# Kernel optimization log

Hardware: AMD Instinct MI355X
Metric: run time of the kernel (lower is better)

Reference implementation:

```python
import jax, jax.numpy as jnp
import numpy as np

N, E, D, H, L, G, C = 50000, 800000, 128, 128, 3, 128, 10
BN_EPS = 1e-5


def setup_inputs() -> dict:
    key = jax.random.key(0)
    ks = jax.random.split(key, 16)
    inp = {
        "x": jax.random.normal(ks[0], (N, D), dtype=jnp.float32),
        "node_centrality": jax.random.uniform(ks[1], (N,), dtype=jnp.float32),
        "edge_centrality": jax.random.uniform(ks[2], (E,), dtype=jnp.float32),
        # stacked per-layer MLP params (in == hidden so stackable)
        "W1": jax.random.normal(ks[3], (L, D, H), dtype=jnp.float32) * 0.05,
        "b1": jnp.zeros((L, H), dtype=jnp.float32),
        "g1": jnp.ones((L, H), dtype=jnp.float32),
        "be1": jnp.zeros((L, H), dtype=jnp.float32),
        "W2": jax.random.normal(ks[4], (L, H, H), dtype=jnp.float32) * 0.05,
        "b2": jnp.zeros((L, H), dtype=jnp.float32),
        "Wc": jax.random.normal(ks[5], (H, C), dtype=jnp.float32) * 0.05,
        "bc": jnp.zeros((C,), dtype=jnp.float32),
        "edge_index": jax.random.randint(ks[6], (2, E), 0, N, dtype=jnp.int64),
        "batch": jnp.sort(jax.random.randint(ks[7], (N,), 0, G, dtype=jnp.int64)),
    }
    return inp


def _gin_forward(x, node_centrality, edge_centrality, W1, b1, g1, be1, W2, b2, Wc, bc, edge_index, batch):
    src, dst = edge_index[0], edge_index[1]  # x_j = x[src], aggregate at dst
    ec = edge_centrality[:, None]
    nc = node_centrality[:, None]
    for l in range(L):
        # message: gather + scale by edge centrality; aggr='add': scatter-add
        msg = x[src] * ec                                      # [E, H]
        agg = jax.ops.segment_sum(msg, dst, num_segments=N)    # [N, H]
        h = agg * nc + x                                       # (1 + eps) * x_r, eps = 0
        # MLP([in, hidden, hidden]): Linear -> BatchNorm(train) -> ReLU -> Linear
        h = h @ W1[l] + b1[l]
        mu = h.mean(axis=0)
        var = h.var(axis=0)  # biased, matches BN training stats
        h = (h - mu) * jax.lax.rsqrt(var + BN_EPS) * g1[l] + be1[l]
        h = jax.nn.relu(h)
        h = h @ W2[l] + b2[l]
        x = jax.nn.relu(h)  # outer .relu() in GIN.forward
    # global mean pool over graphs
    sums = jax.ops.segment_sum(x, batch, num_segments=G)           # [G, H]
    cnt = jax.ops.segment_sum(jnp.ones((N,), x.dtype), batch, num_segments=G)
    pooled = sums / jnp.maximum(cnt, 1.0)[:, None]
    return pooled @ Wc + bc  # [G, C]


def reference(x, edge_index, batch, node_centrality, edge_centrality, W1, b1, g1, be1, W2, b2, Wc, bc):
    return _gin_forward(x, node_centrality, edge_centrality, W1, b1, g1, be1, W2, b2, Wc, bc, edge_index, batch)
```

## Files before the change

### kernel.cpp

```cpp
#include <hip/hip_runtime.h>
#include <hip/hip_fp16.h>

#define Nn 50000
#define Ee 800000
#define HD 128
#define Ll 3
#define Gg 128
#define Cc 10
#define BN_EPS 1e-5f
#define NBLK1 782
#define PPAD 800
#define NSCB 49

typedef __attribute__((ext_vector_type(8))) __bf16 bf16x8;
typedef __attribute__((ext_vector_type(4))) __bf16 bf16x4;
typedef __attribute__((ext_vector_type(4))) float f32x4;

__global__ void k_deg(const int* __restrict__ dst, int* __restrict__ deg) {
  int i = blockIdx.x * blockDim.x + threadIdx.x;
  int base = i * 4;
  if (base >= Ee) return;
#pragma unroll
  for (int j = 0; j < 4; ++j) {
    int e = base + j;
    if (e < Ee) atomicAdd(&deg[dst[e]], 1);
  }
}

__global__ void k_scan1(const int* __restrict__ deg, int* __restrict__ offs,
                        int* __restrict__ bsum) {
  __shared__ int b0[1024], b1[1024];
  int tid = threadIdx.x;
  int i = blockIdx.x * 1024 + tid;
  int v = (i < Nn) ? deg[i] : 0;
  int* cur = b0; int* nxt = b1;
  cur[tid] = v;
  __syncthreads();
  for (int off = 1; off < 1024; off <<= 1) {
    int s = cur[tid] + ((tid >= off) ? cur[tid - off] : 0);
    nxt[tid] = s;
    __syncthreads();
    int* t = cur; cur = nxt; nxt = t;
  }
  if (i < Nn) offs[i] = cur[tid] - v;
  if (tid == 1023) bsum[blockIdx.x] = cur[1023];
}

__global__ void k_scan2(const int* __restrict__ bsum, int* __restrict__ carry) {
  int lane = threadIdx.x;
  int v = (lane < NSCB) ? bsum[lane] : 0;
  int s = v;
  for (int off = 1; off < 64; off <<= 1) {
    int t = __shfl_up(s, off, 64);
    if (lane >= off) s += t;
  }
  if (lane < NSCB) carry[lane] = s - v;
}

__global__ void k_scan3(const int* __restrict__ carry, int* __restrict__ offs,
                        int* __restrict__ cursor) {
  int i = blockIdx.x * 1024 + threadIdx.x;
  if (i < Nn) {
    int o = offs[i] + carry[blockIdx.x];
    offs[i] = o; cursor[i] = o;
  }
  if (i == 0) offs[Nn] = Ee;
}

__global__ void k_fill(const int* __restrict__ src, const int* __restrict__ dst,
                       const float* __restrict__ ec, int* __restrict__ cursor,
                       unsigned int* __restrict__ epk) {
  int i = blockIdx.x * blockDim.x + threadIdx.x;
  int base = i * 4;
  if (base >= Ee) return;
  int d[4], s[4], p[4]; unsigned short hb[4]; bool ok[4];
#pragma unroll
  for (int j = 0; j < 4; ++j) {
    int e = base + j;
    ok[j] = e < Ee;
    if (ok[j]) {
      d[j] = dst[e]; s[j] = src[e];
      hb[j] = __half_as_ushort(__float2half(ec[e]));
    }
  }
#pragma unroll
  for (int j = 0; j < 4; ++j)
    if (ok[j]) p[j] = atomicAdd(&cursor[d[j]], 1);
#pragma unroll
  for (int j = 0; j < 4; ++j)
    if (ok[j]) epk[p[j]] = ((unsigned int)s[j] << 16) | hb[j];
}

__global__ void k_xcast(const float* __restrict__ x, __bf16* __restrict__ xb) {
  int i = blockIdx.x * blockDim.x + threadIdx.x;
  int stride = gridDim.x * blockDim.x;
  const int n4 = Nn * 32;
  for (int t = i; t < n4; t += stride) {
    f32x4 v = ((const f32x4*)x)[t];
    bf16x4 b;
#pragma unroll
    for (int j = 0; j < 4; ++j) b[j] = (__bf16)v[j];
    ((bf16x4*)xb)[t] = b;
  }
}

__global__ void k_wprep(const float* __restrict__ W1, const float* __restrict__ W2,
                        __bf16* __restrict__ wtHi, __bf16* __restrict__ wtLo) {
  int mat = blockIdx.x >> 3;
  int chunk = blockIdx.x & 7;
  const float* W = (mat < 3) ? (W1 + mat * 16384) : (W2 + (mat - 3) * 16384);
  __bf16* hi = wtHi + mat * 16384;
  __bf16* lo = wtLo + mat * 16384;
  for (int t = threadIdx.x; t < 2048; t += blockDim.x) {
    int idx = chunk * 2048 + t;
    int n = idx >> 7, k = idx & 127;
    float v = W[k * 128 + n];
    __bf16 h = (__bf16)v;
    hi[idx] = h;
    lo[idx] = (__bf16)(v - (float)h);
  }
}

__global__ void k_agg(const __bf16* __restrict__ xb, const int* __restrict__ offs,
                      const unsigned int* __restrict__ epk, float* __restrict__ agg) {
  int wid = threadIdx.x >> 6, lane = threadIdx.x & 63;
  int n = blockIdx.x * 4 + wid;
  if (n >= Nn) return;
  int beg = offs[n], end = offs[n + 1];
  const unsigned int* x2 = (const unsigned int*)xb;
  float ax0 = 0.f, ay0 = 0.f, ax1 = 0.f, ay1 = 0.f;
  float ax2 = 0.f, ay2 = 0.f, ax3 = 0.f, ay3 = 0.f;
  int j = beg;
  for (; j + 3 < end; j += 4) {
    unsigned int e0 = epk[j], e1 = epk[j + 1], e2 = epk[j + 2], e3 = epk[j + 3];
    unsigned int v0 = x2[(e0 >> 16) * 64 + lane];
    unsigned int v1 = x2[(e1 >> 16) * 64 + lane];
    unsigned int v2 = x2[(e2 >> 16) * 64 + lane];
    unsigned int v3 = x2[(e3 >> 16) * 64 + lane];
    __half_raw h0, h1, h2, h3;
    h0.x = (unsigned short)(e0 & 0xffffu); h1.x = (unsigned short)(e1 & 0xffffu);
    h2.x = (unsigned short)(e2 & 0xffffu); h3.x = (unsigned short)(e3 & 0xffffu);
    float w0 = __half2float(h0), w1 = __half2float(h1);
    float w2 = __half2float(h2), w3 = __half2float(h3);
    ax0 = fmaf(__uint_as_float(v0 << 16), w0, ax0);
    ay0 = fmaf(__uint_as_float(v0 & 0xffff0000u), w0, ay0);
    ax1 = fmaf(__uint_as_float(v1 << 16), w1, ax1);
    ay1 = fmaf(__uint_as_float(v1 & 0xffff0000u), w1, ay1);
    ax2 = fmaf(__uint_as_float(v2 << 16), w2, ax2);
    ay2 = fmaf(__uint_as_float(v2 & 0xffff0000u), w2, ay2);
    ax3 = fmaf(__uint_as_float(v3 << 16), w3, ax3);
    ay3 = fmaf(__uint_as_float(v3 & 0xffff0000u), w3, ay3);
  }
  for (; j < end; ++j) {
    unsigned int e = epk[j];
    unsigned int v = x2[(e >> 16) * 64 + lane];
    __half_raw h; h.x = (unsigned short)(e & 0xffffu);
    float w = __half2float(h);
    ax0 = fmaf(__uint_as_float(v << 16), w, ax0);
    ay0 = fmaf(__uint_as_float(v & 0xffff0000u), w, ay0);
  }
  float2 acc = make_float2(ax0 + ax1 + ax2 + ax3, ay0 + ay1 + ay2 + ay3);
  ((float2*)agg)[n * 64 + lane] = acc;
}

__device__ __forceinline__ void split8(const float* a, bf16x8& hi, bf16x8& lo) {
#pragma unroll
  for (int j = 0; j < 8; ++j) {
    float v = a[j];
    __bf16 h = (__bf16)v;
    hi[j] = h;
    lo[j] = (__bf16)(v - (float)h);
  }
}

__launch_bounds__(128)
__global__ void k_gemm1(const float* __restrict__ agg, const float* __restrict__ nc,
                        const float* __restrict__ xin,
                        const __bf16* __restrict__ wtHi, const __bf16* __restrict__ wtLo,
                        const float* __restrict__ bias, float* __restrict__ out,
                        float* __restrict__ partial) {
  int tid = threadIdx.x;
  int w = tid >> 6, l = tid & 63;
  int row0 = blockIdx.x * 64;
  int l15 = l & 15, lg = l >> 4;
  int colw = w * 64;
  int krow = lg * 8;

  f32x4 acc[4][4];
#pragma unroll
  for (int m = 0; m < 4; ++m)
#pragma unroll
    for (int n = 0; n < 4; ++n) acc[m][n] = (f32x4){0.f, 0.f, 0.f, 0.f};

  int rowA[4]; bool rv[4]; float ncv[4];
#pragma unroll
  for (int m = 0; m < 4; ++m) {
    rowA[m] = row0 + m * 16 + l15;
    rv[m] = rowA[m] < Nn;
    ncv[m] = rv[m] ? nc[rowA[m]] : 0.f;
  }

#pragma unroll
  for (int ks = 0; ks < 4; ++ks) {
    int k0 = ks * 32 + krow;
    bf16x8 aHi[4], aLo[4];
#pragma unroll
    for (int m = 0; m < 4; ++m) {
      float av[8];
      if (rv[m]) {
        const float* ap = agg + rowA[m] * 128 + k0;
        const float* xp = xin + rowA[m] * 128 + k0;
        f32x4 g0 = *(const f32x4*)ap, g1 = *(const f32x4*)(ap + 4);
        f32x4 x0 = *(const f32x4*)xp, x1 = *(const f32x4*)(xp + 4);
#pragma unroll
        for (int jj = 0; jj < 4; ++jj) {
          av[jj]     = fmaf(g0[jj], ncv[m], x0[jj]);
          av[4 + jj] = fmaf(g1[jj], ncv[m], x1[jj]);
        }
      } else {
#pragma unroll
        for (int jj = 0; jj < 8; ++jj) av[jj] = 0.f;
      }
      split8(av, aHi[m], aLo[m]);
    }
    bf16x8 bHi[4], bLo[4];
#pragma unroll
    for (int n = 0; n < 4; ++n) {
      int c = colw + n * 16 + l15;
      bHi[n] = *(const bf16x8*)(wtHi + c * 128 + k0);
      bLo[n] = *(const bf16x8*)(wtLo + c * 128 + k0);
    }
#pragma unroll
    for (int m = 0; m < 4; ++m)
#pragma unroll
      for (int n = 0; n < 4; ++n) {
        acc[m][n] = __builtin_amdgcn_mfma_f32_16x16x32_bf16(aHi[m], bHi[n], acc[m][n], 0, 0, 0);
        acc[m][n] = __builtin_amdgcn_mfma_f32_16x16x32_bf16(aLo[m], bHi[n], acc[m][n], 0, 0, 0);
        acc[m][n] = __builtin_amdgcn_mfma_f32_16x16x32_bf16(aHi[m], bLo[n], acc[m][n], 0, 0, 0);
      }
  }

  float s[4] = {0.f, 0.f, 0.f, 0.f}, q[4] = {0.f, 0.f, 0.f, 0.f};
#pragma unroll
  for (int n = 0; n < 4; ++n) {
    int c = colw + n * 16 + l15;
    float bv = bias[c];
#pragma unroll
    for (int m = 0; m < 4; ++m) {
      int rbase = row0 + m * 16 + lg * 4;
#pragma unroll
      for (int r = 0; r < 4; ++r) {
        int rr = rbase + r;
        if (rr < Nn) {
          float o = acc[m][n][r] + bv;
          out[rr * 128 + c] = o;
          s[n] += o; q[n] += o * o;
        }
      }
    }
  }
#pragma unroll
  for (int n = 0; n < 4; ++n) {
    s[n] += __shfl_xor(s[n], 16, 64); q[n] += __shfl_xor(q[n], 16, 64);
    s[n] += __shfl_xor(s[n], 32, 64); q[n] += __shfl_xor(q[n], 32, 64);
  }
  if (lg == 0) {
    int blk = blockIdx.x;
#pragma unroll
    for (int n = 0; n < 4; ++n) {
      int f = colw + n * 16 + l15;
      partial[f * PPAD + blk] = s[n];
      partial[(128 + f) * PPAD + blk] = q[n];
    }
  }
}

__global__ void k_bnfin(const float* __restrict__ partial,
                        const float* __restrict__ g1, const float* __restrict__ be1,
                        float* __restrict__ scaleA, float* __restrict__ shiftA) {
  __shared__ float ss[256], qq[256];
  int f = blockIdx.x, t = threadIdx.x;
  float s = 0.f, q = 0.f;
  for (int b = t; b < NBLK1; b += 256) {
    s += partial[f * PPAD + b];
    q += partial[(128 + f) * PPAD + b];
  }
  ss[t] = s; qq[t] = q;
  __syncthreads();
  for (int off = 128; off > 0; off >>= 1) {
    if (t < off) { ss[t] += ss[t + off]; qq[t] += qq[t + off]; }
    __syncthreads();
  }
  if (t == 0) {
    const float inv = 1.0f / (float)Nn;
    float mu = ss[0] * inv;
    float var = fmaxf(qq[0] * inv - mu * mu, 0.f);
    float rs = rsqrtf(var + BN_EPS);
    float sc = rs * g1[f];
    scaleA[f] = sc;
    shiftA[f] = be1[f] - mu * sc;
  }
}

__launch_bounds__(128)
__global__ void k_gemm2(const float* __restrict__ h1, const float* __restrict__ scaleA,
                        const float* __restrict__ shiftA,
                        const __bf16* __restrict__ wtHi, const __bf16* __restrict__ wtLo,
                        const float* __restrict__ bias, float* __restrict__ out,
                        __bf16* __restrict__ xbout) {
  int tid = threadIdx.x;
  int w = tid >> 6, l = tid & 63;
  int row0 = blockIdx.x * 64;
  int l15 = l & 15, lg = l >> 4;
  int colw = w * 64;
  int krow = lg * 8;

  f32x4 acc[4][4];
#pragma unroll
  for (int m = 0; m < 4; ++m)
#pragma unroll
    for (int n = 0; n < 4; ++n) acc[m][n] = (f32x4){0.f, 0.f, 0.f, 0.f};

  int rowA[4]; bool rv[4];
#pragma unroll
  for (int m = 0; m < 4; ++m) {
    rowA[m] = row0 + m * 16 + l15;
    rv[m] = rowA[m] < Nn;
  }

#pragma unroll
  for (int ks = 0; ks < 4; ++ks) {
    int k0 = ks * 32 + krow;
    f32x4 sc0 = *(const f32x4*)(scaleA + k0), sc1 = *(const f32x4*)(scaleA + k0 + 4);
    f32x4 sh0 = *(const f32x4*)(shiftA + k0), sh1 = *(const f32x4*)(shiftA + k0 + 4);
    bf16x8 aHi[4], aLo[4];
#pragma unroll
    for (int m = 0; m < 4; ++m) {
      float av[8];
      if (rv[m]) {
        const float* hp = h1 + rowA[m] * 128 + k0;
        f32x4 h0 = *(const f32x4*)hp, h1v = *(const f32x4*)(hp + 4);
#pragma unroll
        for (int jj = 0; jj < 4; ++jj) {
          av[jj]     = fmaxf(fmaf(h0[jj],  sc0[jj], sh0[jj]), 0.f);
          av[4 + jj] = fmaxf(fmaf(h1v[jj], sc1[jj], sh1[jj]), 0.f);
        }
      } else {
#pragma unroll
        for (int jj = 0; jj < 8; ++jj) av[jj] = 0.f;
      }
      split8(av, aHi[m], aLo[m]);
    }
    bf16x8 bHi[4], bLo[4];
#pragma unroll
    for (int n = 0; n < 4; ++n) {
      int c = colw + n * 16 + l15;
      bHi[n] = *(const bf16x8*)(wtHi + c * 128 + k0);
      bLo[n] = *(const bf16x8*)(wtLo + c * 128 + k0);
    }
#pragma unroll
    for (int m = 0; m < 4; ++m)
#pragma unroll
      for (int n = 0; n < 4; ++n) {
        acc[m][n] = __builtin_amdgcn_mfma_f32_16x16x32_bf16(aHi[m], bHi[n], acc[m][n], 0, 0, 0);
        acc[m][n] = __builtin_amdgcn_mfma_f32_16x16x32_bf16(aLo[m], bHi[n], acc[m][n], 0, 0, 0);
        acc[m][n] = __builtin_amdgcn_mfma_f32_16x16x32_bf16(aHi[m], bLo[n], acc[m][n], 0, 0, 0);
      }
  }

#pragma unroll
  for (int n = 0; n < 4; ++n) {
    int c = colw + n * 16 + l15;
    float bv = bias[c];
#pragma unroll
    for (int m = 0; m < 4; ++m) {
      int rbase = row0 + m * 16 + lg * 4;
#pragma unroll
      for (int r = 0; r < 4; ++r) {
        int rr = rbase + r;
        if (rr < Nn) {
          float o = fmaxf(acc[m][n][r] + bv, 0.f);
          out[rr * 128 + c] = o;
          xbout[rr * 128 + c] = (__bf16)o;
        }
      }
    }
  }
}

#define PCH 64
__global__ void k_pool(const float* __restrict__ xin, const int* __restrict__ batch,
                       float* __restrict__ pooled, float* __restrict__ gcnt) {
  int wid = threadIdx.x >> 6, lane = threadIdx.x & 63;
  int w = blockIdx.x * 4 + wid;
  int n0 = w * PCH;
  if (n0 >= Nn) return;
  int n1 = (n0 + PCH < Nn) ? n0 + PCH : Nn;
  const float2* x2 = (const float2*)xin;
  float2 acc = make_float2(0.f, 0.f);
  int cur = batch[n0];
  int cnt = 0;
  for (int n = n0; n < n1; ++n) {
    int g = batch[n];
    if (g != cur) {
      atomicAdd(&pooled[cur * 128 + lane * 2 + 0], acc.x);
      atomicAdd(&pooled[cur * 128 + lane * 2 + 1], acc.y);
      if (lane == 0) atomicAdd(&gcnt[cur], (float)cnt);
      acc = make_float2(0.f, 0.f); cnt = 0; cur = g;
    }
    float2 v = x2[n * 64 + lane];
    acc.x += v.x; acc.y += v.y; ++cnt;
  }
  atomicAdd(&pooled[cur * 128 + lane * 2 + 0], acc.x);
  atomicAdd(&pooled[cur * 128 + lane * 2 + 1], acc.y);
  if (lane == 0) atomicAdd(&gcnt[cur], (float)cnt);
}

__global__ void k_head(const float* __restrict__ pooled, const float* __restrict__ gcnt,
                       const float* __restrict__ Wc, const float* __restrict__ bc,
                       float* __restrict__ out) {
  __shared__ float p[128];
  int g = blockIdx.x, tid = threadIdx.x;
  p[tid] = pooled[g * 128 + tid] / fmaxf(gcnt[g], 1.0f);
  __syncthreads();
  if (tid < Cc) {
    float acc = bc[tid];
    for (int k = 0; k < 128; ++k) acc = fmaf(p[k], Wc[k * Cc + tid], acc);
    out[g * Cc + tid] = acc;
  }
}

extern "C" void kernel_launch(void* const* d_in, const int* in_sizes, int n_in,
                              void* d_out, int out_size, void* d_ws, size_t ws_size,
                              hipStream_t stream) {
  const float* x    = (const float*)d_in[0];
  const float* ncn  = (const float*)d_in[1];
  const float* ecn  = (const float*)d_in[2];
  const float* W1   = (const float*)d_in[3];
  const float* b1   = (const float*)d_in[4];
  const float* g1   = (const float*)d_in[5];
  const float* be1  = (const float*)d_in[6];
  const float* W2   = (const float*)d_in[7];
  const float* b2   = (const float*)d_in[8];
  const float* Wc   = (const float*)d_in[9];
  const float* bc   = (const float*)d_in[10];
  const int*   ei   = (const int*)d_in[11];
  const int*   batch= (const int*)d_in[12];
  const int* src  = ei;
  const int* dstp = ei + Ee;

  float* fws = (float*)d_ws;
  float* bufA     = fws;
  float* bufB     = fws +  6400000;
  float* h1       = fws + 12800000;
  float* partial  = fws + 19200000;
  float* scaleA   = partial + 256 * PPAD;
  float* shiftA   = scaleA + 128;
  float* pooled   = shiftA + 128;
  float* gcnt     = pooled + Gg * 128;
  int*   ib       = (int*)(gcnt + 128);
  int*   deg      = ib;
  int*   offs     = deg + Nn;
  int*   cursor   = offs + Nn + 64;
  int*   bsum     = cursor + Nn;
  int*   carry    = bsum + 64;
  unsigned int* epk = (unsigned int*)(carry + 64);
  __bf16* wtHi    = (__bf16*)(epk + Ee);
  __bf16* wtLo    = wtHi + 6 * 16384;
  __bf16* xb      = wtLo + 6 * 16384;

  k_wprep<<<48, 256, 0, stream>>>(W1, W2, wtHi, wtLo);
  k_xcast<<<2048, 256, 0, stream>>>(x, xb);
  hipMemsetAsync(deg, 0, Nn * sizeof(int), stream);
  k_deg<<<(Ee / 4 + 255) / 256, 256, 0, stream>>>(dstp, deg);
  k_scan1<<<NSCB, 1024, 0, stream>>>(deg, offs, bsum);
  k_scan2<<<1, 64, 0, stream>>>(bsum, carry);
  k_scan3<<<NSCB, 1024, 0, stream>>>(carry, offs, cursor);
  k_fill<<<(Ee / 4 + 255) / 256, 256, 0, stream>>>(src, dstp, ecn, cursor, epk);

  const float* xin = x;
  for (int l = 0; l < Ll; ++l) {
    float* aggb = (l & 1) ? bufB : bufA;
    k_agg<<<(Nn + 3) / 4, 256, 0, stream>>>(xb, offs, epk, aggb);
    k_gemm1<<<NBLK1, 128, 0, stream>>>(aggb, ncn, xin,
                                       wtHi + l * 16384, wtLo + l * 16384,
                                       b1 + l * 128, h1, partial);
    k_bnfin<<<128, 256, 0, stream>>>(partial, g1 + l * 128, be1 + l * 128,
                                     scaleA, shiftA);
    k_gemm2<<<NBLK1, 128, 0, stream>>>(h1, scaleA, shiftA,
                                       wtHi + (3 + l) * 16384, wtLo + (3 + l) * 16384,
                                       b2 + l * 128, aggb, xb);
    xin = aggb;
  }

  hipMemsetAsync(pooled, 0, (Gg * 128 + 128) * sizeof(float), stream);
  k_pool<<<(Nn + PCH * 4 - 1) / (PCH * 4), 256, 0, stream>>>(xin, batch, pooled, gcnt);
  k_head<<<Gg, 128, 0, stream>>>(pooled, gcnt, Wc, bc, (float*)d_out);
}
```

Before: 536.6 us.

## Drop fp32 node-feature copy, use bf16 x everywhere; split GEMM blocks across 4 waves

```diff
diff --git a/kernel.cpp b/kernel.cpp
--- a/kernel.cpp
+++ b/kernel.cpp
@@ -9,7 +9,8 @@
 #define Cc 10
 #define BN_EPS 1e-5f
 #define NBLK1 782
-#define PPAD 800
+#define NPART 1564
+#define PPAD 1600
 #define NSCB 49
 
 typedef __attribute__((ext_vector_type(8))) __bf16 bf16x8;
@@ -173,28 +174,29 @@
   }
 }
 
-__launch_bounds__(128)
+__launch_bounds__(256)
 __global__ void k_gemm1(const float* __restrict__ agg, const float* __restrict__ nc,
-                        const float* __restrict__ xin,
+                        const __bf16* __restrict__ xb,
                         const __bf16* __restrict__ wtHi, const __bf16* __restrict__ wtLo,
                         const float* __restrict__ bias, float* __restrict__ out,
                         float* __restrict__ partial) {
   int tid = threadIdx.x;
   int w = tid >> 6, l = tid & 63;
-  int row0 = blockIdx.x * 64;
+  int wr = w >> 1, wc = w & 1;
+  int row0 = blockIdx.x * 64 + wr * 32;
   int l15 = l & 15, lg = l >> 4;
-  int colw = w * 64;
+  int colw = wc * 64;
   int krow = lg * 8;
 
-  f32x4 acc[4][4];
-#pragma unroll
-  for (int m = 0; m < 4; ++m)
+  f32x4 acc[2][4];
+#pragma unroll
+  for (int m = 0; m < 2; ++m)
 #pragma unroll
     for (int n = 0; n < 4; ++n) acc[m][n] = (f32x4){0.f, 0.f, 0.f, 0.f};
 
-  int rowA[4]; bool rv[4]; float ncv[4];
-#pragma unroll
-  for (int m = 0; m < 4; ++m) {
+  int rowA[2]; bool rv[2]; float ncv[2];
+#pragma unroll
+  for (int m = 0; m < 2; ++m) {
     rowA[m] = row0 + m * 16 + l15;
     rv[m] = rowA[m] < Nn;
     ncv[m] = rv[m] ? nc[rowA[m]] : 0.f;
@@ -203,19 +205,18 @@
 #pragma unroll
   for (int ks = 0; ks < 4; ++ks) {
     int k0 = ks * 32 + krow;
-    bf16x8 aHi[4], aLo[4];
-#pragma unroll
-    for (int m = 0; m < 4; ++m) {
+    bf16x8 aHi[2], aLo[2];
+#pragma unroll
+    for (int m = 0; m < 2; ++m) {
       float av[8];
       if (rv[m]) {
         const float* ap = agg + rowA[m] * 128 + k0;
-        const float* xp = xin + rowA[m] * 128 + k0;
+        bf16x8 xv = *(const bf16x8*)(xb + rowA[m] * 128 + k0);
         f32x4 g0 = *(const f32x4*)ap, g1 = *(const f32x4*)(ap + 4);
-        f32x4 x0 = *(const f32x4*)xp, x1 = *(const f32x4*)(xp + 4);
 #pragma unroll
         for (int jj = 0; jj < 4; ++jj) {
-          av[jj]     = fmaf(g0[jj], ncv[m], x0[jj]);
-          av[4 + jj] = fmaf(g1[jj], ncv[m], x1[jj]);
+          av[jj]     = fmaf(g0[jj], ncv[m], (float)xv[jj]);
+          av[4 + jj] = fmaf(g1[jj], ncv[m], (float)xv[4 + jj]);
         }
       } else {
 #pragma unroll
@@ -231,7 +232,7 @@
       bLo[n] = *(const bf16x8*)(wtLo + c * 128 + k0);
     }
 #pragma unroll
-    for (int m = 0; m < 4; ++m)
+    for (int m = 0; m < 2; ++m)
 #pragma unroll
       for (int n = 0; n < 4; ++n) {
         acc[m][n] = __builtin_amdgcn_mfma_f32_16x16x32_bf16(aHi[m], bHi[n], acc[m][n], 0, 0, 0);
@@ -246,7 +247,7 @@
     int c = colw + n * 16 + l15;
     float bv = bias[c];
 #pragma unroll
-    for (int m = 0; m < 4; ++m) {
+    for (int m = 0; m < 2; ++m) {
       int rbase = row0 + m * 16 + lg * 4;
 #pragma unroll
       for (int r = 0; r < 4; ++r) {
@@ -265,12 +266,12 @@
     s[n] += __shfl_xor(s[n], 32, 64); q[n] += __shfl_xor(q[n], 32, 64);
   }
   if (lg == 0) {
-    int blk = blockIdx.x;
+    int slot = blockIdx.x * 2 + wr;
 #pragma unroll
     for (int n = 0; n < 4; ++n) {
       int f = colw + n * 16 + l15;
-      partial[f * PPAD + blk] = s[n];
-      partial[(128 + f) * PPAD + blk] = q[n];
+      partial[f * PPAD + slot] = s[n];
+      partial[(128 + f) * PPAD + slot] = q[n];
     }
   }
 }
@@ -281,7 +282,7 @@
   __shared__ float ss[256], qq[256];
   int f = blockIdx.x, t = threadIdx.x;
   float s = 0.f, q = 0.f;
-  for (int b = t; b < NBLK1; b += 256) {
+  for (int b = t; b < NPART; b += 256) {
     s += partial[f * PPAD + b];
     q += partial[(128 + f) * PPAD + b];
   }
@@ -302,28 +303,28 @@
   }
 }
 
-__launch_bounds__(128)
+__launch_bounds__(256)
 __global__ void k_gemm2(const float* __restrict__ h1, const float* __restrict__ scaleA,
                         const float* __restrict__ shiftA,
                         const __bf16* __restrict__ wtHi, const __bf16* __restrict__ wtLo,
-                        const float* __restrict__ bias, float* __restrict__ out,
-                        __bf16* __restrict__ xbout) {
+                        const float* __restrict__ bias, __bf16* __restrict__ xbout) {
   int tid = threadIdx.x;
   int w = tid >> 6, l = tid & 63;
-  int row0 = blockIdx.x * 64;
+  int wr = w >> 1, wc = w & 1;
+  int row0 = blockIdx.x * 64 + wr * 32;
   int l15 = l & 15, lg = l >> 4;
-  int colw = w * 64;
+  int colw = wc * 64;
   int krow = lg * 8;
 
-  f32x4 acc[4][4];
-#pragma unroll
-  for (int m = 0; m < 4; ++m)
+  f32x4 acc[2][4];
+#pragma unroll
+  for (int m = 0; m < 2; ++m)
 #pragma unroll
     for (int n = 0; n < 4; ++n) acc[m][n] = (f32x4){0.f, 0.f, 0.f, 0.f};
 
-  int rowA[4]; bool rv[4];
-#pragma unroll
-  for (int m = 0; m < 4; ++m) {
+  int rowA[2]; bool rv[2];
+#pragma unroll
+  for (int m = 0; m < 2; ++m) {
     rowA[m] = row0 + m * 16 + l15;
     rv[m] = rowA[m] < Nn;
   }
@@ -333,9 +334,9 @@
     int k0 = ks * 32 + krow;
     f32x4 sc0 = *(const f32x4*)(scaleA + k0), sc1 = *(const f32x4*)(scaleA + k0 + 4);
     f32x4 sh0 = *(const f32x4*)(shiftA + k0), sh1 = *(const f32x4*)(shiftA + k0 + 4);
-    bf16x8 aHi[4], aLo[4];
-#pragma unroll
-    for (int m = 0; m < 4; ++m) {
+    bf16x8 aHi[2], aLo[2];
+#pragma unroll
+    for (int m = 0; m < 2; ++m) {
       float av[8];
       if (rv[m]) {
         const float* hp = h1 + rowA[m] * 128 + k0;
@@ -359,7 +360,7 @@
       bLo[n] = *(const bf16x8*)(wtLo + c * 128 + k0);
     }
 #pragma unroll
-    for (int m = 0; m < 4; ++m)
+    for (int m = 0; m < 2; ++m)
 #pragma unroll
       for (int n = 0; n < 4; ++n) {
         acc[m][n] = __builtin_amdgcn_mfma_f32_16x16x32_bf16(aHi[m], bHi[n], acc[m][n], 0, 0, 0);
@@ -373,30 +374,26 @@
     int c = colw + n * 16 + l15;
     float bv = bias[c];
 #pragma unroll
-    for (int m = 0; m < 4; ++m) {
+    for (int m = 0; m < 2; ++m) {
       int rbase = row0 + m * 16 + lg * 4;
 #pragma unroll
       for (int r = 0; r < 4; ++r) {
         int rr = rbase + r;
-        if (rr < Nn) {
-          float o = fmaxf(acc[m][n][r] + bv, 0.f);
-          out[rr * 128 + c] = o;
-          xbout[rr * 128 + c] = (__bf16)o;
-        }
+        if (rr < Nn) xbout[rr * 128 + c] = (__bf16)fmaxf(acc[m][n][r] + bv, 0.f);
       }
     }
   }
 }
 
 #define PCH 64
-__global__ void k_pool(const float* __restrict__ xin, const int* __restrict__ batch,
+__global__ void k_pool(const __bf16* __restrict__ xb, const int* __restrict__ batch,
                        float* __restrict__ pooled, float* __restrict__ gcnt) {
   int wid = threadIdx.x >> 6, lane = threadIdx.x & 63;
   int w = blockIdx.x * 4 + wid;
   int n0 = w * PCH;
   if (n0 >= Nn) return;
   int n1 = (n0 + PCH < Nn) ? n0 + PCH : Nn;
-  const float2* x2 = (const float2*)xin;
+  const unsigned int* x2 = (const unsigned int*)xb;
   float2 acc = make_float2(0.f, 0.f);
   int cur = batch[n0];
   int cnt = 0;
@@ -408,8 +405,10 @@
       if (lane == 0) atomicAdd(&gcnt[cur], (float)cnt);
       acc = make_float2(0.f, 0.f); cnt = 0; cur = g;
     }
-    float2 v = x2[n * 64 + lane];
-    acc.x += v.x; acc.y += v.y; ++cnt;
+    unsigned int v = x2[n * 64 + lane];
+    acc.x += __uint_as_float(v << 16);
+    acc.y += __uint_as_float(v & 0xffff0000u);
+    ++cnt;
   }
   atomicAdd(&pooled[cur * 128 + lane * 2 + 0], acc.x);
   atomicAdd(&pooled[cur * 128 + lane * 2 + 1], acc.y);
@@ -450,16 +449,14 @@
   const int* dstp = ei + Ee;
 
   float* fws = (float*)d_ws;
-  float* bufA     = fws;
-  float* bufB     = fws +  6400000;
-  float* h1       = fws + 12800000;
-  float* partial  = fws + 19200000;
+  float* agg      = fws;
+  float* h1       = fws +  6400000;
+  float* partial  = fws + 12800000;
   float* scaleA   = partial + 256 * PPAD;
   float* shiftA   = scaleA + 128;
   float* pooled   = shiftA + 128;
   float* gcnt     = pooled + Gg * 128;
-  int*   ib       = (int*)(gcnt + 128);
-  int*   deg      = ib;
+  int*   deg      = (int*)(gcnt + 128);
   int*   offs     = deg + Nn;
   int*   cursor   = offs + Nn + 64;
   int*   bsum     = cursor + Nn;
@@ -478,22 +475,19 @@
   k_scan3<<<NSCB, 1024, 0, stream>>>(carry, offs, cursor);
   k_fill<<<(Ee / 4 + 255) / 256, 256, 0, stream>>>(src, dstp, ecn, cursor, epk);
 
-  const float* xin = x;
   for (int l = 0; l < Ll; ++l) {
-    float* aggb = (l & 1) ? bufB : bufA;
-    k_agg<<<(Nn + 3) / 4, 256, 0, stream>>>(xb, offs, epk, aggb);
-    k_gemm1<<<NBLK1, 128, 0, stream>>>(aggb, ncn, xin,
+    k_agg<<<(Nn + 3) / 4, 256, 0, stream>>>(xb, offs, epk, agg);
+    k_gemm1<<<NBLK1, 256, 0, stream>>>(agg, ncn, xb,
                                        wtHi + l * 16384, wtLo + l * 16384,
                                        b1 + l * 128, h1, partial);
     k_bnfin<<<128, 256, 0, stream>>>(partial, g1 + l * 128, be1 + l * 128,
                                      scaleA, shiftA);
-    k_gemm2<<<NBLK1, 128, 0, stream>>>(h1, scaleA, shiftA,
+    k_gemm2<<<NBLK1, 256, 0, stream>>>(h1, scaleA, shiftA,
                                        wtHi + (3 + l) * 16384, wtLo + (3 + l) * 16384,
-                                       b2 + l * 128, aggb, xb);
-    xin = aggb;
+                                       b2 + l * 128, xb);
   }
 
   hipMemsetAsync(pooled, 0, (Gg * 128 + 128) * sizeof(float), stream);
-  k_pool<<<(Nn + PCH * 4 - 1) / (PCH * 4), 256, 0, stream>>>(xin, batch, pooled, gcnt);
+  k_pool<<<(Nn + PCH * 4 - 1) / (PCH * 4), 256, 0, stream>>>(xb, batch, pooled, gcnt);
   k_head<<<Gg, 128, 0, stream>>>(pooled, gcnt, Wc, bc, (float*)d_out);
 }
```

Measured after the change: 553.3 us. 3.1% more time.
